# Optimization experiments

Measured on AMD Instinct MI355X. Metric: run time of the kernel, lower is better.

The kernel has to match this reference:

```python
import jax, jax.numpy as jnp
import numpy as np
from jax import lax

D_MODEL, D_STATE, D_CONV, EXPAND = 1024, 16, 4, 2
D_INNER = EXPAND * D_MODEL
B, L = 2, 2048


def setup_inputs() -> dict:
    key = jax.random.key(0)
    ks = jax.random.split(key, 8)
    s_in = 1.0 / np.sqrt(D_MODEL)
    s_xp = 1.0 / np.sqrt(D_INNER)
    x = jax.random.normal(ks[0], (B, L, D_MODEL), dtype=jnp.float32)
    W_in = jax.random.uniform(ks[1], (2 * D_INNER, D_MODEL), minval=-s_in, maxval=s_in)
    conv_w = jax.random.uniform(ks[2], (D_INNER, 1, D_CONV), minval=-0.5, maxval=0.5)
    conv_b = jax.random.uniform(ks[3], (D_INNER,), minval=-0.5, maxval=0.5)
    W_xproj = jax.random.uniform(ks[4], (1 + 2 * D_STATE, D_INNER), minval=-s_xp, maxval=s_xp)
    W_dt = jax.random.uniform(ks[5], (D_INNER, 1), minval=-1.0, maxval=1.0)
    b_dt = jax.random.uniform(ks[6], (D_INNER,), minval=-1.0, maxval=1.0)
    A_log = jnp.log(jnp.broadcast_to(jnp.arange(1, D_STATE + 1, dtype=jnp.float32), (D_INNER, D_STATE)))
    D = jnp.ones((D_INNER,), dtype=jnp.float32)
    W_out = jax.random.uniform(ks[7], (D_MODEL, D_INNER), minval=-s_xp, maxval=s_xp)
    return {"x": x, "W_in": W_in, "conv_w": conv_w, "conv_b": conv_b,
            "W_xproj": W_xproj, "W_dt": W_dt, "b_dt": b_dt,
            "A_log": A_log, "D": D, "W_out": W_out}


def reference(x, W_in, conv_w, conv_b, W_xproj, W_dt, b_dt, A_log, D, W_out):
    b, l, _ = x.shape
    d_state = A_log.shape[1]
    d_conv = conv_w.shape[-1]

    xz = x @ W_in.T                                  # (B, L, 2*d_inner)
    x_in, z = jnp.split(xz, 2, axis=-1)

    # causal depthwise conv: torch pads both sides then truncates to [:L]
    lhs = jnp.pad(x_in.transpose(0, 2, 1), ((0, 0), (0, 0), (d_conv - 1, 0)))  # (B, d_inner, L+pad)
    conv = lax.conv_general_dilated(
        lhs, conv_w, window_strides=(1,), padding='VALID',
        dimension_numbers=('NCW', 'OIW', 'NCW'),
        feature_group_count=conv_w.shape[0])
    x_conv = jax.nn.silu(conv.transpose(0, 2, 1) + conv_b)  # (B, L, d_inner)

    ssm_in = x_conv @ W_xproj.T                      # (B, L, 1+2*d_state)
    dt_raw = ssm_in[..., :1]
    B_ssm = ssm_in[..., 1:1 + d_state]               # (B, L, d_state)
    C_ssm = ssm_in[..., 1 + d_state:]                # (B, L, d_state)

    delta = jax.nn.softplus(dt_raw @ W_dt.T + b_dt)  # (B, L, d_inner)
    A = -jnp.exp(A_log)                              # (d_inner, d_state)
    deltaA = jnp.exp(delta[..., None] * A)           # (B, L, d_inner, d_state)
    deltaB_u = delta[..., None] * B_ssm[:, :, None, :] * x_conv[..., None]

    def step(h, inp):
        dA, dBu, c = inp                              # (B,d_inner,d_state)x2, (B,d_state)
        h = dA * h + dBu
        y = jnp.einsum('bds,bs->bd', h, c)
        return h, y

    h0 = jnp.zeros((b, deltaA.shape[2], d_state), dtype=x.dtype)
    _, ys = lax.scan(step, h0, (deltaA.transpose(1, 0, 2, 3),
                                deltaB_u.transpose(1, 0, 2, 3),
                                C_ssm.transpose(1, 0, 2)))
    y = ys.transpose(1, 0, 2) + x_conv * D           # (B, L, d_inner)
    y = y * jax.nn.silu(z)
    return y @ W_out.T
```

## Files before the change

kernel.cpp:

```cpp
#include <hip/hip_runtime.h>
#include <hip/hip_bf16.h>
#include <math.h>

#define D_MODEL 1024
#define D_STATE 16
#define D_CONV  4
#define D_INNER 2048
#define BB      2
#define LL      2048
#define BLROWS  (BB*LL)
#define NCHUNK  64
#define CHUNK   (LL/NCHUNK)
#define SSML    36
#define XSPLIT  16

typedef __hip_bfloat16 bf16;
typedef __attribute__((ext_vector_type(8))) short short8;
typedef __attribute__((ext_vector_type(4))) float f32x4;

__device__ __forceinline__ float ldf(const void* p, long i, int isbf) {
    return isbf ? __bfloat162float(((const bf16*)p)[i]) : ((const float*)p)[i];
}
__device__ __forceinline__ short bfbits(float f) {
    bf16 h = __float2bfloat16(f);
    return *(short*)&h;
}
__device__ __forceinline__ float bits2f(short s) {
    bf16 h; *(short*)&h = s; return __bfloat162float(h);
}
__device__ __forceinline__ float bf2f(bf16 h) { return __bfloat162float(h); }
__device__ __forceinline__ float siluf(float x) {
    return __fdividef(x, 1.f + __expf(-x));
}
__device__ __forceinline__ void softplus_r(float x, float& delta, float& r) {
    float e = __expf(-fabsf(x));
    float t = 1.f + e;
    delta = fmaxf(x, 0.f) + __logf(t);
    r = __fdividef((x >= 0.f) ? e : 1.f, t);
}

#define OFF_CW   0
#define OFF_CB   8192
#define OFF_WDT  10240
#define OFF_BDT  12288
#define OFF_AA   14336
#define OFF_D    47104
#define N_SMALL  49152
#define N_WXPB   (128*2048)
#define N_SSMZ   (BLROWS*SSML)

__global__ void dtype_probe(const unsigned short* __restrict__ alog, int* __restrict__ flag) {
    if (threadIdx.x == 0) { flag[0] = (alog[1] != 0) ? 1 : 0; flag[1] = 1; }
}

__global__ __launch_bounds__(256) void cvt_prep(
    const void* __restrict__ Wxp, const void* __restrict__ cw,
    const void* __restrict__ cb, const void* __restrict__ wdt,
    const void* __restrict__ bdt, const void* __restrict__ alog,
    const void* __restrict__ Dp,
    bf16* __restrict__ wxpb, float* __restrict__ smallf,
    float* __restrict__ ssm, int* __restrict__ flag)
{
    const int isbf = flag[0];
    int idx = blockIdx.x * 256 + threadIdx.x;
    if (idx < N_WXPB) {
        int row = idx >> 11, col = idx & 2047;
        float v = (row < 33) ? ldf(Wxp, (long)row*2048 + col, isbf) : 0.f;
        wxpb[idx] = __float2bfloat16(v);
        return;
    }
    int j = idx - N_WXPB;
    if      (j < 8192)  smallf[OFF_CW  + j]         = ldf(cw,  j, isbf);
    else if (j < 10240) smallf[OFF_CB  + j - 8192]  = ldf(cb,  j - 8192, isbf);
    else if (j < 12288) smallf[OFF_WDT + j - 10240] = ldf(wdt, j - 10240, isbf);
    else if (j < 14336) smallf[OFF_BDT + j - 12288] = ldf(bdt, j - 12288, isbf);
    else if (j < 47104) {
        int jj = j - 14336;
        float aa = -__expf(ldf(alog, jj, isbf));
        smallf[OFF_AA + jj] = aa;
        int s = jj & 15;
        if (fabsf(aa + (float)(s+1)) > 1e-3f) flag[1] = 0;
    }
    else if (j < 49152) smallf[OFF_D   + j - 47104] = ldf(Dp,  j - 47104, isbf);
    else {
        int z = j - N_SMALL;
        if (z < N_SSMZ) ssm[z] = 0.f;
    }
}

__global__ __launch_bounds__(256) void cvt_all(
    const void* __restrict__ x, const void* __restrict__ win,
    const void* __restrict__ wout,
    bf16* __restrict__ xb, bf16* __restrict__ winb, bf16* __restrict__ woutb,
    const int* __restrict__ flagp)
{
    const int isbf = *flagp;
    int i = blockIdx.x * 256 + threadIdx.x;
    const void* src; bf16* dst; long o;
    if (i < 524288)       { src = x;    dst = xb;    o = (long)i * 8; }
    else if (i < 1048576) { src = win;  dst = winb;  o = (long)(i - 524288) * 8; }
    else if (i < 1310720) { src = wout; dst = woutb; o = (long)(i - 1048576) * 8; }
    else return;
    short8 v;
    if (isbf) {
        v = *(const short8*)((const bf16*)src + o);
    } else {
        const float* s = (const float*)src + o;
        f32x4 u = *(const f32x4*)s, w = *(const f32x4*)(s + 4);
        v[0]=bfbits(u[0]); v[1]=bfbits(u[1]); v[2]=bfbits(u[2]); v[3]=bfbits(u[3]);
        v[4]=bfbits(w[0]); v[5]=bfbits(w[1]); v[6]=bfbits(w[2]); v[7]=bfbits(w[3]);
    }
    *(short8*)(dst + o) = v;
}

__global__ __launch_bounds__(256) void gemm_dual(
    const void* __restrict__ A, int lda,
    const void* __restrict__ Bm, int ldb,
    void* __restrict__ Cp, int ldc, int K,
    const int* __restrict__ flagp, int amode, int bmode, int cmode)
{
    const int isbf = *flagp;
    const int a_bf = amode ? isbf : 1;
    const int b_bf = bmode ? isbf : 1;
    const int c_bf = cmode ? isbf : 1;

    __shared__ bf16 As[128*64];
    __shared__ bf16 Bs[128*64];
    const int t    = threadIdx.x;
    const int lane = t & 63;
    const int w    = t >> 6;
    const int wm   = w >> 1, wn = w & 1;
    const int bm   = blockIdx.y, bn = blockIdx.x;
    const int quad = lane >> 4, l16 = lane & 15;

    f32x4 acc[4][4];
    #pragma unroll
    for (int i = 0; i < 4; i++)
        #pragma unroll
        for (int j = 0; j < 4; j++)
            acc[i][j] = f32x4{0.f, 0.f, 0.f, 0.f};

    for (int k0 = 0; k0 < K; k0 += 64) {
        __syncthreads();
        if (a_bf) {
            #pragma unroll
            for (int seg = 0; seg < 4; seg++) {
                int s = seg*256 + t, row = s >> 3, sg = s & 7;
                int col = (sg ^ (row & 7)) * 8;
                const bf16* ga = (const bf16*)A + ((long)bm*128 + row)*(long)lda + k0 + col;
                __builtin_amdgcn_global_load_lds(
                    (const __attribute__((address_space(1))) void*)ga,
                    (__attribute__((address_space(3))) void*)&As[row*64 + sg*8], 16, 0, 0);
            }
        } else {
            #pragma unroll
            for (int seg = 0; seg < 4; seg++) {
                int s = seg*256 + t, row = s >> 3, sg = s & 7;
                int col = (sg ^ (row & 7)) * 8;
                const float* ap = (const float*)A + ((long)bm*128 + row)*(long)lda + k0 + col;
                f32x4 u = *(const f32x4*)ap, v = *(const f32x4*)(ap + 4);
                short8 va;
                va[0]=bfbits(u[0]); va[1]=bfbits(u[1]); va[2]=bfbits(u[2]); va[3]=bfbits(u[3]);
                va[4]=bfbits(v[0]); va[5]=bfbits(v[1]); va[6]=bfbits(v[2]); va[7]=bfbits(v[3]);
                *(short8*)&As[row*64 + sg*8] = va;
            }
        }
        if (b_bf) {
            #pragma unroll
            for (int seg = 0; seg < 4; seg++) {
                int s = seg*256 + t, row = s >> 3, sg = s & 7;
                int col = (sg ^ (row & 7)) * 8;
                const bf16* gb = (const bf16*)Bm + ((long)bn*128 + row)*(long)ldb + k0 + col;
                __builtin_amdgcn_global_load_lds(
                    (const __attribute__((address_space(1))) void*)gb,
                    (__attribute__((address_space(3))) void*)&Bs[row*64 + sg*8], 16, 0, 0);
            }
        } else {
            #pragma unroll
            for (int seg = 0; seg < 4; seg++) {
                int s = seg*256 + t, row = s >> 3, sg = s & 7;
                int col = (sg ^ (row & 7)) * 8;
                const float* bp = (const float*)Bm + ((long)bn*128 + row)*(long)ldb + k0 + col;
                f32x4 u = *(const f32x4*)bp, v = *(const f32x4*)(bp + 4);
                short8 vb;
                vb[0]=bfbits(u[0]); vb[1]=bfbits(u[1]); vb[2]=bfbits(u[2]); vb[3]=bfbits(u[3]);
                vb[4]=bfbits(v[0]); vb[5]=bfbits(v[1]); vb[6]=bfbits(v[2]); vb[7]=bfbits(v[3]);
                *(short8*)&Bs[row*64 + sg*8] = vb;
            }
        }
        __syncthreads();

        #pragma unroll
        for (int kk = 0; kk < 64; kk += 32) {
            const int cbase = kk >> 3;
            short8 af[4], bfr[4];
            #pragma unroll
            for (int mi = 0; mi < 4; mi++) {
                int row = wm*64 + mi*16 + l16;
                int c = cbase + quad;
                af[mi] = *(const short8*)&As[row*64 + ((c ^ (row & 7))*8)];
            }
            #pragma unroll
            for (int ni = 0; ni < 4; ni++) {
                int row = wn*64 + ni*16 + l16;
                int c = cbase + quad;
                bfr[ni] = *(const short8*)&Bs[row*64 + ((c ^ (row & 7))*8)];
            }
            #pragma unroll
            for (int mi = 0; mi < 4; mi++)
                #pragma unroll
                for (int ni = 0; ni < 4; ni++)
                    acc[mi][ni] = __builtin_amdgcn_mfma_f32_16x16x32_bf16(
                        af[mi], bfr[ni], acc[mi][ni], 0, 0, 0);
        }
    }

    #pragma unroll
    for (int mi = 0; mi < 4; mi++)
        #pragma unroll
        for (int ni = 0; ni < 4; ni++)
            #pragma unroll
            for (int r = 0; r < 4; r++) {
                int row = bm*128 + wm*64 + mi*16 + quad*4 + r;
                int col = bn*128 + wn*64 + ni*16 + l16;
                float val = acc[mi][ni][r];
                if (c_bf) ((bf16*)Cp)[(long)row * ldc + col] = __float2bfloat16(val);
                else      ((float*)Cp)[(long)row * ldc + col] = val;
            }
}

__global__ __launch_bounds__(256) void gemm_n64(
    const bf16* __restrict__ A, int lda,
    const void* __restrict__ Bm, int ldb,
    void* __restrict__ Cp, int ldc, int K,
    const int* __restrict__ flagp, int bmode, int cmode)
{
    const int isbf = *flagp;
    const int b_bf = bmode ? isbf : 1;
    const int c_bf = cmode ? isbf : 1;

    __shared__ bf16 As[128*64];
    __shared__ bf16 Bs[64*64];
    const int t    = threadIdx.x;
    const int lane = t & 63;
    const int w    = t >> 6;
    const int wm   = w >> 1, wn = w & 1;
    const int bm   = blockIdx.y, bn = blockIdx.x;
    const int quad = lane >> 4, l16 = lane & 15;

    f32x4 acc[4][2];
    #pragma unroll
    for (int i = 0; i < 4; i++)
        #pragma unroll
        for (int j = 0; j < 2; j++)
            acc[i][j] = f32x4{0.f, 0.f, 0.f, 0.f};

    for (int k0 = 0; k0 < K; k0 += 64) {
        __syncthreads();
        #pragma unroll
        for (int seg = 0; seg < 4; seg++) {
            int s = seg*256 + t, row = s >> 3, sg = s & 7;
            int col = (sg ^ (row & 7)) * 8;
            const bf16* ga = A + ((long)bm*128 + row)*(long)lda + k0 + col;
            __builtin_amdgcn_global_load_lds(
                (const __attribute__((address_space(1))) void*)ga,
                (__attribute__((address_space(3))) void*)&As[row*64 + sg*8], 16, 0, 0);
        }
        if (b_bf) {
            #pragma unroll
            for (int seg = 0; seg < 2; seg++) {
                int s = seg*256 + t, row = s >> 3, sg = s & 7;
                int col = (sg ^ (row & 7)) * 8;
                const bf16* gb = (const bf16*)Bm + ((long)bn*64 + row)*(long)ldb + k0 + col;
                __builtin_amdgcn_global_load_lds(
                    (const __attribute__((address_space(1))) void*)gb,
                    (__attribute__((address_space(3))) void*)&Bs[row*64 + sg*8], 16, 0, 0);
            }
        } else {
            #pragma unroll
            for (int seg = 0; seg < 2; seg++) {
                int s = seg*256 + t, row = s >> 3, sg = s & 7;
                int col = (sg ^ (row & 7)) * 8;
                const float* bp = (const float*)Bm + ((long)bn*64 + row)*(long)ldb + k0 + col;
                f32x4 u = *(const f32x4*)bp, v = *(const f32x4*)(bp + 4);
                short8 vb;
                vb[0]=bfbits(u[0]); vb[1]=bfbits(u[1]); vb[2]=bfbits(u[2]); vb[3]=bfbits(u[3]);
                vb[4]=bfbits(v[0]); vb[5]=bfbits(v[1]); vb[6]=bfbits(v[2]); vb[7]=bfbits(v[3]);
                *(short8*)&Bs[row*64 + sg*8] = vb;
            }
        }
        __syncthreads();

        #pragma unroll
        for (int kk = 0; kk < 64; kk += 32) {
            const int cbase = kk >> 3;
            short8 af[4], bfr[2];
            #pragma unroll
            for (int mi = 0; mi < 4; mi++) {
                int row = wm*64 + mi*16 + l16;
                int c = cbase + quad;
                af[mi] = *(const short8*)&As[row*64 + ((c ^ (row & 7))*8)];
            }
            #pragma unroll
            for (int ni = 0; ni < 2; ni++) {
                int row = wn*32 + ni*16 + l16;
                int c = cbase + quad;
                bfr[ni] = *(const short8*)&Bs[row*64 + ((c ^ (row & 7))*8)];
            }
            #pragma unroll
            for (int mi = 0; mi < 4; mi++)
                #pragma unroll
                for (int ni = 0; ni < 2; ni++)
                    acc[mi][ni] = __builtin_amdgcn_mfma_f32_16x16x32_bf16(
                        af[mi], bfr[ni], acc[mi][ni], 0, 0, 0);
        }
    }

    #pragma unroll
    for (int mi = 0; mi < 4; mi++)
        #pragma unroll
        for (int ni = 0; ni < 2; ni++)
            #pragma unroll
            for (int r = 0; r < 4; r++) {
                int row = bm*128 + wm*64 + mi*16 + quad*4 + r;
                int col = bn*64 + wn*32 + ni*16 + l16;
                float val = acc[mi][ni][r];
                if (c_bf) ((bf16*)Cp)[(long)row * ldc + col] = __float2bfloat16(val);
                else      ((float*)Cp)[(long)row * ldc + col] = val;
            }
}

__global__ __launch_bounds__(256) void xproj_fused(
    const bf16* __restrict__ xz, const bf16* __restrict__ wxpb,
    const float* __restrict__ smallf, float* __restrict__ ssm)
{
    const float* cwf = smallf + OFF_CW;
    const float* cbf = smallf + OFF_CB;
    __shared__ bf16 As[128*32];
    __shared__ bf16 Bs[128*32];
    const int t    = threadIdx.x;
    const int lane = t & 63;
    const int w    = t >> 6;
    const int wm   = w >> 1, wn = w & 1;
    const int bm   = blockIdx.y;
    const int ks   = blockIdx.x * (D_INNER / XSPLIT);
    const int quad = lane >> 4, l16 = lane & 15;

    f32x4 acc[4][4];
    #pragma unroll
    for (int i = 0; i < 4; i++)
        #pragma unroll
        for (int j = 0; j < 4; j++)
            acc[i][j] = f32x4{0.f, 0.f, 0.f, 0.f};

    for (int k0 = ks; k0 < ks + D_INNER/XSPLIT; k0 += 32) {
        __syncthreads();
        #pragma unroll
        for (int seg = 0; seg < 2; seg++) {
            int s = seg*256 + t, row = s >> 2, dcol = (s & 3) * 8;
            int blg = bm*128 + row;
            int b = blg >> 11, l = blg & (LL - 1);
            int d0 = k0 + dcol;
            float a[8];
            {
                f32x4 c0 = *(const f32x4*)&cbf[d0], c1 = *(const f32x4*)&cbf[d0+4];
                a[0]=c0[0]; a[1]=c0[1]; a[2]=c0[2]; a[3]=c0[3];
                a[4]=c1[0]; a[5]=c1[1]; a[6]=c1[2]; a[7]=c1[3];
            }
            f32x4 cw4[8];
            #pragma unroll
            for (int j = 0; j < 8; j++) cw4[j] = *(const f32x4*)&cwf[(d0+j)*4];
            #pragma unroll
            for (int kk = 0; kk < D_CONV; kk++) {
                int ls = l - 3 + kk;
                if (ls >= 0) {
                    short8 xv = *(const short8*)&xz[((long)(b*LL + ls))*4096 + d0];
                    #pragma unroll
                    for (int j = 0; j < 8; j++) a[j] += bits2f(xv[j]) * cw4[j][kk];
                }
            }
            short8 va;
            #pragma unroll
            for (int j = 0; j < 8; j++) va[j] = bfbits(siluf(a[j]));
            *(short8*)&As[row*32 + dcol] = va;
        }
        #pragma unroll
        for (int seg = 0; seg < 2; seg++) {
            int s = seg*256 + t, row = s >> 2, col = (s & 3) * 8;
            const bf16* gb = wxpb + (long)row*D_INNER + k0 + col;
            __builtin_amdgcn_global_load_lds(
                (const __attribute__((address_space(1))) void*)gb,
                (__attribute__((address_space(3))) void*)&Bs[row*32 + col], 16, 0, 0);
        }
        __syncthreads();

        short8 af[4], bfr[4];
        #pragma unroll
        for (int mi = 0; mi < 4; mi++)
            af[mi] = *(const short8*)&As[(wm*64 + mi*16 + l16)*32 + quad*8];
        #pragma unroll
        for (int ni = 0; ni < 4; ni++)
            bfr[ni] = *(const short8*)&Bs[(wn*64 + ni*16 + l16)*32 + quad*8];
        #pragma unroll
        for (int mi = 0; mi < 4; mi++)
            #pragma unroll
            for (int ni = 0; ni < 4; ni++)
                acc[mi][ni] = __builtin_amdgcn_mfma_f32_16x16x32_bf16(
                    af[mi], bfr[ni], acc[mi][ni], 0, 0, 0);
    }

    #pragma unroll
    for (int mi = 0; mi < 4; mi++)
        #pragma unroll
        for (int ni = 0; ni < 4; ni++) {
            int col = wn*64 + ni*16 + l16;
            if (col < 33) {
                int newcol = (col == 0) ? 32 : (col - 1);
                #pragma unroll
                for (int r = 0; r < 4; r++) {
                    int row = bm*128 + wm*64 + mi*16 + quad*4 + r;
                    atomicAdd(&ssm[(long)row * SSML + newcol], acc[mi][ni][r]);
                }
            }
        }
}

template<int CHUNK_T>
__global__ __launch_bounds__(256) void scan_partA(
    const float* __restrict__ ssm, const bf16* __restrict__ xz,
    const float* __restrict__ smallf,
    float* __restrict__ sumdq, float* __restrict__ Q,
    const int* __restrict__ flag)
{
    __shared__ float sL[CHUNK_T*SSML];
    __shared__ bf16  sX[CHUNK_T*256];
    const int fastA = flag[1];
    int d = blockIdx.x * 256 + threadIdx.x;
    int c = blockIdx.y, b = blockIdx.z;
    const int NC = gridDim.y;
    int l0 = c * CHUNK_T;
    {
        const float* src = ssm + (long)(b*LL + l0) * SSML;
        for (int idx = threadIdx.x; idx < CHUNK_T*SSML; idx += 256) sL[idx] = src[idx];
        const bf16* xsrc = xz + (long)(b*LL + l0)*4096 + blockIdx.x*256;
        for (int j = threadIdx.x; j < CHUNK_T*32; j += 256) {
            int li = j >> 5, ln = j & 31;
            *(short8*)&sX[li*256 + ln*8] = *(const short8*)&xsrc[(long)li*4096 + ln*8];
        }
    }
    f32x4 h4[4];
    #pragma unroll
    for (int g = 0; g < 4; g++) h4[g] = f32x4{0.f, 0.f, 0.f, 0.f};
    float Aa[D_STATE];
    if (!fastA) {
        #pragma unroll
        for (int s = 0; s < D_STATE; s++) Aa[s] = smallf[OFF_AA + d*D_STATE + s];
    }
    f32x4 cw4 = *(const f32x4*)&smallf[OFF_CW + d*4];
    float cbv  = smallf[OFF_CB + d];
    float wdt  = smallf[OFF_WDT + d];
    float bdtv = smallf[OFF_BDT + d];
    float win[3];
    #pragma unroll
    for (int k = 0; k < 3; k++) {
        int ls = l0 - 3 + k;
        win[k] = (ls >= 0) ? bf2f(xz[((long)(b*LL + ls))*4096 + d]) : 0.f;
    }
    __syncthreads();
    float sumd = 0.f;
    #pragma unroll 4
    for (int li = 0; li < CHUNK_T; li++) {
        float xnew = bf2f(sX[li*256 + threadIdx.x]);
        float convv = cbv + win[0]*cw4[0] + win[1]*cw4[1] + win[2]*cw4[2] + xnew*cw4[3];
        win[0] = win[1]; win[1] = win[2]; win[2] = xnew;
        float xc = siluf(convv);
        const float* row = &sL[li*SSML];
        f32x4 Bv[4];
        #pragma unroll
        for (int g = 0; g < 4; g++) Bv[g] = *(const f32x4*)(row + g*4);
        float delta, r;
        softplus_r(row[32]*wdt + bdtv, delta, r);
        sumd += delta;
        float du = delta * xc;
        if (fastA) {
            float r2 = r*r;
            float r3 = r2*r;
            float r4 = r2*r2;
            f32x4 p0; p0[0]=r; p0[1]=r2; p0[2]=r3; p0[3]=r4;
            float s8  = r4*r4;
            float s12 = s8*r4;
            h4[0] = p0*h4[0]       + du*Bv[0];
            h4[1] = (p0*r4)*h4[1]  + du*Bv[1];
            h4[2] = (p0*s8)*h4[2]  + du*Bv[2];
            h4[3] = (p0*s12)*h4[3] + du*Bv[3];
        } else {
            #pragma unroll
            for (int g = 0; g < 4; g++)
                #pragma unroll
                for (int j = 0; j < 4; j++) {
                    int s = g*4 + j;
                    h4[g][j] = __expf(delta*Aa[s])*h4[g][j] + du*Bv[g][j];
                }
        }
    }
    sumdq[(long)(b*NC + c)*D_INNER + d] = sumd;
    long o = ((long)(b*NC + c)*D_STATE)*D_INNER + d;
    #pragma unroll
    for (int s = 0; s < D_STATE; s++)
        Q[o + (long)s*D_INNER] = h4[s >> 2][s & 3];
}

__global__ __launch_bounds__(256) void scan_combine(
    const float* __restrict__ sumdq, float* __restrict__ Q_hst,
    const float* __restrict__ smallf, int NC)
{
    int t = blockIdx.x * 256 + threadIdx.x;
    int d = t & (D_INNER - 1);
    int s = (t >> 11) & (D_STATE - 1);
    int b = t >> 15;
    float Aa = smallf[OFF_AA + d*D_STATE + s];
    float h = 0.f;
    #pragma unroll 4
    for (int c = 0; c < NC; c++) {
        float sd = sumdq[(long)(b*NC + c)*D_INNER + d];
        long idx = ((long)(b*NC + c)*D_STATE + s)*D_INNER + d;
        float q = Q_hst[idx];
        Q_hst[idx] = h;
        h = __expf(Aa*sd)*h + q;
    }
}

template<int CHUNK_T>
__global__ __launch_bounds__(256) void scan_partC(
    const float* __restrict__ ssm, bf16* __restrict__ xz,
    const float* __restrict__ smallf, const float* __restrict__ hst,
    const int* __restrict__ flag)
{
    __shared__ float sL[CHUNK_T*SSML];
    __shared__ bf16  sX[CHUNK_T*256];
    __shared__ bf16  sZ[CHUNK_T*256];
    const int fastA = flag[1];
    int d = blockIdx.x * 256 + threadIdx.x;
    int c = blockIdx.y, b = blockIdx.z;
    const int NC = gridDim.y;
    int l0 = c * CHUNK_T;
    {
        const float* src = ssm + (long)(b*LL + l0) * SSML;
        for (int idx = threadIdx.x; idx < CHUNK_T*SSML; idx += 256) sL[idx] = src[idx];
        const bf16* xsrc = xz + (long)(b*LL + l0)*4096 + blockIdx.x*256;
        for (int j = threadIdx.x; j < CHUNK_T*32; j += 256) {
            int li = j >> 5, ln = j & 31;
            *(short8*)&sX[li*256 + ln*8] = *(const short8*)&xsrc[(long)li*4096 + ln*8];
            *(short8*)&sZ[li*256 + ln*8] = *(const short8*)&xsrc[(long)li*4096 + D_INNER + ln*8];
        }
    }
    f32x4 h4[4];
    long o = ((long)(b*NC + c)*D_STATE)*D_INNER + d;
    #pragma unroll
    for (int s = 0; s < D_STATE; s++) h4[s >> 2][s & 3] = hst[o + (long)s*D_INNER];
    float Aa[D_STATE];
    if (!fastA) {
        #pragma unroll
        for (int s = 0; s < D_STATE; s++) Aa[s] = smallf[OFF_AA + d*D_STATE + s];
    }
    f32x4 cw4 = *(const f32x4*)&smallf[OFF_CW + d*4];
    float cbv  = smallf[OFF_CB + d];
    float wdt  = smallf[OFF_WDT + d];
    float bdtv = smallf[OFF_BDT + d];
    float Dv   = smallf[OFF_D + d];
    float win[3];
    #pragma unroll
    for (int k = 0; k < 3; k++) {
        int ls = l0 - 3 + k;
        win[k] = (ls >= 0) ? bf2f(xz[((long)(b*LL + ls))*4096 + d]) : 0.f;
    }
    __syncthreads();
    #pragma unroll 2
    for (int li = 0; li < CHUNK_T; li++) {
        long bl = (long)(b*LL + l0 + li);
        float xnew = bf2f(sX[li*256 + threadIdx.x]);
        float convv = cbv + win[0]*cw4[0] + win[1]*cw4[1] + win[2]*cw4[2] + xnew*cw4[3];
        win[0] = win[1]; win[1] = win[2]; win[2] = xnew;
        float xc = siluf(convv);
        const float* row = &sL[li*SSML];
        f32x4 Bv[4], Cv[4];
        #pragma unroll
        for (int g = 0; g < 4; g++) {
            Bv[g] = *(const f32x4*)(row + g*4);
            Cv[g] = *(const f32x4*)(row + 16 + g*4);
        }
        float delta, r;
        softplus_r(row[32]*wdt + bdtv, delta, r);
        float du = delta * xc;
        f32x4 yacc = f32x4{0.f, 0.f, 0.f, 0.f};
        if (fastA) {
            float r2 = r*r;
            float r3 = r2*r;
            float r4 = r2*r2;
            f32x4 p0; p0[0]=r; p0[1]=r2; p0[2]=r3; p0[3]=r4;
            float s8  = r4*r4;
            float s12 = s8*r4;
            h4[0] = p0*h4[0]       + du*Bv[0];
            h4[1] = (p0*r4)*h4[1]  + du*Bv[1];
            h4[2] = (p0*s8)*h4[2]  + du*Bv[2];
            h4[3] = (p0*s12)*h4[3] + du*Bv[3];
            yacc = yacc + h4[0]*Cv[0];
            yacc = yacc + h4[1]*Cv[1];
            yacc = yacc + h4[2]*Cv[2];
            yacc = yacc + h4[3]*Cv[3];
        } else {
            #pragma unroll
            for (int g = 0; g < 4; g++)
                #pragma unroll
                for (int j = 0; j < 4; j++) {
                    int s = g*4 + j;
                    h4[g][j] = __expf(delta*Aa[s])*h4[g][j] + du*Bv[g][j];
                    yacc[j] += h4[g][j]*Cv[g][j];
                }
        }
        float yv = (yacc[0] + yacc[1]) + (yacc[2] + yacc[3]);
        yv += xc * Dv;
        float z = bf2f(sZ[li*256 + threadIdx.x]);
        yv *= siluf(z);
        xz[bl*4096 + D_INNER + d] = __float2bfloat16(yv);
    }
}

extern "C" void kernel_launch(void* const* d_in, const int* in_sizes, int n_in,
                              void* d_out, int out_size, void* d_ws, size_t ws_size,
                              hipStream_t stream)
{
    char* ws = (char*)d_ws;
    bf16*  xz     = (bf16*) (ws);
    bf16*  wxpb   = (bf16*) (ws + 33554432);
    float* ssm    = (float*)(ws + 34078720);
    float* sumdq  = (float*)(ws + 34668544);
    float* Q      = (float*)(ws + 35717120);
    float* smallf = (float*)(ws + 52494336);
    int*   flag   = (int*)  (ws + 52690944);
    bf16*  woutb  = (bf16*) (ws + 52691008);
    bf16*  xb     = (bf16*) (ws + 35717120);
    bf16*  winb   = (bf16*) (ws + 35717120 + 8388608);
    const bool big = ws_size >= 56885312;

    dtype_probe<<<1, 64, 0, stream>>>((const unsigned short*)d_in[7], flag);

    cvt_prep<<<(N_WXPB + N_SMALL + N_SSMZ)/256, 256, 0, stream>>>(
        d_in[4], d_in[2], d_in[3], d_in[5], d_in[6], d_in[7], d_in[8],
        wxpb, smallf, ssm, flag);

    if (big) {
        cvt_all<<<1310720/256, 256, 0, stream>>>(
            d_in[0], d_in[1], d_in[9], xb, winb, woutb, flag);
        gemm_dual<<<dim3(32, 32), 256, 0, stream>>>(
            xb, D_MODEL, winb, D_MODEL, xz, 2*D_INNER, D_MODEL, flag, 0, 0, 0);
    } else {
        gemm_dual<<<dim3(32, 32), 256, 0, stream>>>(
            d_in[0], D_MODEL, d_in[1], D_MODEL, xz, 2*D_INNER, D_MODEL, flag, 1, 1, 0);
    }

    xproj_fused<<<dim3(XSPLIT, 32), 256, 0, stream>>>(xz, wxpb, smallf, ssm);

    {
        dim3 g(D_INNER/256, NCHUNK, BB);
        scan_partA<CHUNK><<<g, 256, 0, stream>>>(ssm, xz, smallf, sumdq, Q, flag);
        scan_combine<<<(BB*D_STATE*D_INNER)/256, 256, 0, stream>>>(sumdq, Q, smallf, NCHUNK);
        scan_partC<CHUNK><<<g, 256, 0, stream>>>(ssm, xz, smallf, Q, flag);
    }

    if (big) {
        gemm_n64<<<dim3(D_MODEL/64, 32), 256, 0, stream>>>(
            xz + D_INNER, 2*D_INNER, woutb, D_INNER, d_out, D_MODEL, D_INNER, flag, 0, 1);
    } else {
        gemm_n64<<<dim3(D_MODEL/64, 32), 256, 0, stream>>>(
            xz + D_INNER, 2*D_INNER, d_in[9], D_INNER, d_out, D_MODEL, D_INNER, flag, 1, 1);
    }
}
```

Baseline: 292.2 us.

## Add double-buffered 256x256 tile GEMM for input projection

Replaces the 128x128 single-buffered in_proj GEMM on the bf16 path with a new 512-thread kernel that uses 256x256 output tiles and two LDS buffers. It prefetches two K-tiles ahead with global_load_lds, coordinated by explicit vmcnt waits and barriers, and raises wave priority around the MFMA block. This is meant to overlap global loads with matrix math and raise arithmetic intensity per block. In exchange it needs 128KB of LDS and many accumulator registers, and launches only 256 blocks, which risks low occupancy or spills.

Measured after the change: 289.2 us. No clear change (-1.0%).

```diff
diff --git a/kernel.cpp b/kernel.cpp
--- a/kernel.cpp
+++ b/kernel.cpp
@@ -48,6 +48,10 @@
 #define N_SMALL  49152
 #define N_WXPB   (128*2048)
 #define N_SSMZ   (BLROWS*SSML)
+
+#define G_LDS16(gptr, lptr) __builtin_amdgcn_global_load_lds( \
+    (const __attribute__((address_space(1))) void*)(gptr),    \
+    (__attribute__((address_space(3))) void*)(lptr), 16, 0, 0)
 
 __global__ void dtype_probe(const unsigned short* __restrict__ alog, int* __restrict__ flag) {
     if (threadIdx.x == 0) { flag[0] = (alog[1] != 0) ? 1 : 0; flag[1] = 1; }
@@ -113,6 +117,101 @@
     *(short8*)(dst + o) = v;
 }
 
+__global__ __launch_bounds__(512) void gemm8p(
+    const bf16* __restrict__ A,
+    const bf16* __restrict__ Bm,
+    bf16* __restrict__ Cp)
+{
+    __shared__ bf16 As[2][256*64];
+    __shared__ bf16 Bs[2][256*64];
+    const int t    = threadIdx.x;
+    const int lane = t & 63;
+    const int wm   = (t >> 6) >> 2;
+    const int wn   = (t >> 6) & 3;
+    const int bm   = blockIdx.y, bn = blockIdx.x;
+    const int quad = lane >> 4, l16 = lane & 15;
+    const int NST  = 16;
+
+    f32x4 acc[8][4];
+    #pragma unroll
+    for (int i = 0; i < 8; i++)
+        #pragma unroll
+        for (int j = 0; j < 4; j++)
+            acc[i][j] = f32x4{0.f, 0.f, 0.f, 0.f};
+
+    auto stage = [&](int bufi, int kt) {
+        #pragma unroll
+        for (int seg = 0; seg < 4; seg++) {
+            int s = seg*512 + t, row = s >> 3, sg = s & 7;
+            int col = (sg ^ (row & 7)) * 8;
+            G_LDS16(A + ((long)bm*256 + row)*1024 + kt*64 + col, &As[bufi][s*8]);
+        }
+        #pragma unroll
+        for (int seg = 0; seg < 4; seg++) {
+            int s = seg*512 + t, row = s >> 3, sg = s & 7;
+            int col = (sg ^ (row & 7)) * 8;
+            G_LDS16(Bm + ((long)bn*256 + row)*1024 + kt*64 + col, &Bs[bufi][s*8]);
+        }
+    };
+
+    stage(0, 0);
+    stage(1, 1);
+    asm volatile("s_waitcnt vmcnt(8)" ::: "memory");
+    __builtin_amdgcn_s_barrier();
+
+    int cur = 0;
+    for (int t0 = 0; t0 < NST; ++t0) {
+        short8 af[2][8], bfv[2][4];
+        #pragma unroll
+        for (int kk = 0; kk < 2; kk++) {
+            #pragma unroll
+            for (int rt = 0; rt < 8; rt++) {
+                int row = wm*128 + rt*16 + l16;
+                int c = kk*4 + quad;
+                af[kk][rt] = *(const short8*)&As[cur][row*64 + ((c ^ (row & 7))*8)];
+            }
+            #pragma unroll
+            for (int ct = 0; ct < 4; ct++) {
+                int row = wn*64 + ct*16 + l16;
+                int c = kk*4 + quad;
+                bfv[kk][ct] = *(const short8*)&Bs[cur][row*64 + ((c ^ (row & 7))*8)];
+            }
+        }
+        asm volatile("s_waitcnt lgkmcnt(0)" ::: "memory");
+        __builtin_amdgcn_sched_barrier(0);
+        __builtin_amdgcn_s_barrier();
+        __builtin_amdgcn_sched_barrier(0);
+        if (t0 + 2 < NST) stage(cur, t0 + 2);
+        __builtin_amdgcn_s_setprio(1);
+        #pragma unroll
+        for (int kk = 0; kk < 2; kk++)
+            #pragma unroll
+            for (int rt = 0; rt < 8; rt++)
+                #pragma unroll
+                for (int ct = 0; ct < 4; ct++)
+                    acc[rt][ct] = __builtin_amdgcn_mfma_f32_16x16x32_bf16(
+                        af[kk][rt], bfv[kk][ct], acc[rt][ct], 0, 0, 0);
+        __builtin_amdgcn_s_setprio(0);
+        __builtin_amdgcn_sched_barrier(0);
+        if (t0 + 2 < NST) { asm volatile("s_waitcnt vmcnt(8)" ::: "memory"); }
+        else              { asm volatile("s_waitcnt vmcnt(0)" ::: "memory"); }
+        __builtin_amdgcn_sched_barrier(0);
+        __builtin_amdgcn_s_barrier();
+        cur ^= 1;
+    }
+
+    #pragma unroll
+    for (int rt = 0; rt < 8; rt++)
+        #pragma unroll
+        for (int ct = 0; ct < 4; ct++)
+            #pragma unroll
+            for (int r = 0; r < 4; r++) {
+                int row = bm*256 + wm*128 + rt*16 + quad*4 + r;
+                int col = bn*256 + wn*64 + ct*16 + l16;
+                Cp[(long)row * 4096 + col] = __float2bfloat16(acc[rt][ct][r]);
+            }
+}
+
 __global__ __launch_bounds__(256) void gemm_dual(
     const void* __restrict__ A, int lda,
     const void* __restrict__ Bm, int ldb,
@@ -148,9 +247,7 @@
                 int s = seg*256 + t, row = s >> 3, sg = s & 7;
                 int col = (sg ^ (row & 7)) * 8;
                 const bf16* ga = (const bf16*)A + ((long)bm*128 + row)*(long)lda + k0 + col;
-                __builtin_amdgcn_global_load_lds(
-                    (const __attribute__((address_space(1))) void*)ga,
-                    (__attribute__((address_space(3))) void*)&As[row*64 + sg*8], 16, 0, 0);
+                G_LDS16(ga, &As[row*64 + sg*8]);
             }
         } else {
             #pragma unroll
@@ -171,9 +268,7 @@
                 int s = seg*256 + t, row = s >> 3, sg = s & 7;
                 int col = (sg ^ (row & 7)) * 8;
                 const bf16* gb = (const bf16*)Bm + ((long)bn*128 + row)*(long)ldb + k0 + col;
-                __builtin_amdgcn_global_load_lds(
-                    (const __attribute__((address_space(1))) void*)gb,
-                    (__attribute__((address_space(3))) void*)&Bs[row*64 + sg*8], 16, 0, 0);
+                G_LDS16(gb, &Bs[row*64 + sg*8]);
             }
         } else {
             #pragma unroll
@@ -262,9 +357,7 @@
             int s = seg*256 + t, row = s >> 3, sg = s & 7;
             int col = (sg ^ (row & 7)) * 8;
             const bf16* ga = A + ((long)bm*128 + row)*(long)lda + k0 + col;
-            __builtin_amdgcn_global_load_lds(
-                (const __attribute__((address_space(1))) void*)ga,
-                (__attribute__((address_space(3))) void*)&As[row*64 + sg*8], 16, 0, 0);
+            G_LDS16(ga, &As[row*64 + sg*8]);
         }
         if (b_bf) {
             #pragma unroll
@@ -272,9 +365,7 @@
                 int s = seg*256 + t, row = s >> 3, sg = s & 7;
                 int col = (sg ^ (row & 7)) * 8;
                 const bf16* gb = (const bf16*)Bm + ((long)bn*64 + row)*(long)ldb + k0 + col;
-                __builtin_amdgcn_global_load_lds(
-                    (const __attribute__((address_space(1))) void*)gb,
-                    (__attribute__((address_space(3))) void*)&Bs[row*64 + sg*8], 16, 0, 0);
+                G_LDS16(gb, &Bs[row*64 + sg*8]);
             }
         } else {
             #pragma unroll
@@ -388,9 +479,7 @@
         for (int seg = 0; seg < 2; seg++) {
             int s = seg*256 + t, row = s >> 2, col = (s & 3) * 8;
             const bf16* gb = wxpb + (long)row*D_INNER + k0 + col;
-            __builtin_amdgcn_global_load_lds(
-                (const __attribute__((address_space(1))) void*)gb,
-                (__attribute__((address_space(3))) void*)&Bs[row*32 + col], 16, 0, 0);
+            G_LDS16(gb, &Bs[row*32 + col]);
         }
         __syncthreads();
 
@@ -652,8 +741,7 @@
     if (big) {
         cvt_all<<<1310720/256, 256, 0, stream>>>(
             d_in[0], d_in[1], d_in[9], xb, winb, woutb, flag);
-        gemm_dual<<<dim3(32, 32), 256, 0, stream>>>(
-            xb, D_MODEL, winb, D_MODEL, xz, 2*D_INNER, D_MODEL, flag, 0, 0, 0);
+        gemm8p<<<dim3(16, 16), 512, 0, stream>>>(xb, winb, xz);
     } else {
         gemm_dual<<<dim3(32, 32), 256, 0, stream>>>(
             d_in[0], D_MODEL, d_in[1], D_MODEL, xz, 2*D_INNER, D_MODEL, flag, 1, 1, 0);
```
